# Kernel tuning notes

Hardware: AMD Instinct MI355X
Metric: run time of the kernel (lower is better)

The kernel has to match this reference:

```python
import jax, jax.numpy as jnp
import numpy as np

BINS = 30
MOMENTUM = 0.75
LOSS_WEIGHT = 1.0


def setup_inputs() -> dict:
    key = jax.random.key(0)
    k1, k2 = jax.random.split(key)
    N, C = 8192, 2048
    preds = jax.random.normal(k1, (N, C), dtype=jnp.float32)
    targets = jax.random.randint(k2, (N, C), 0, 2).astype(jnp.int32)  # binary multi-hot
    acc_sum = jnp.zeros((BINS, C), dtype=jnp.float32)  # EMA histogram state
    return {"preds": preds, "targets": targets, "acc_sum": acc_sum}


def reference(preds, targets, acc_sum):
    N, C = preds.shape
    t = targets.astype(preds.dtype)

    # gradient norm g = |sigmoid(p) - t|, detached (weights carry no grad)
    g = jnp.abs(jax.nn.sigmoid(jax.lax.stop_gradient(preds)) - t)

    # bin index: edges[i] = i/BINS, so bin = floor(g*BINS), g=1.0 -> last bin (edge[-1]+=1e-6)
    bin_idx = jnp.clip(jnp.floor(g * BINS).astype(jnp.int32), 0, BINS - 1)  # [N, C]

    # per-label histogram: counts[b, c] = #examples with bin b in column c
    cols = jnp.broadcast_to(jnp.arange(C, dtype=jnp.int32)[None, :], (N, C))
    counts = jnp.zeros((BINS, C), dtype=preds.dtype).at[bin_idx, cols].add(1.0)

    # n[c] = number of non-empty bins for label c
    n = jnp.sum(counts >= 1.0, axis=0).astype(preds.dtype)  # [C]

    # EMA update of the histogram (momentum > 0 branch)
    acc_new = MOMENTUM * acc_sum + (1.0 - MOMENTUM) * counts  # [BINS, C]

    tot = jnp.asarray(float(max(N, 1.0)), preds.dtype)
    weights = tot / acc_new[bin_idx, cols]               # gather per-element density
    weights = weights / jnp.maximum(n, 1.0)[None, :]      # normalize by #valid bins
    weights = jax.lax.stop_gradient(weights)

    # BCE with logits, elementwise: softplus-style stable form
    bce = jnp.logaddexp(0.0, preds) - preds * t
    loss = jnp.mean(weights * bce)
    return loss * LOSS_WEIGHT
```

## Files before the change

kernel.cpp:

```cpp
#include <hip/hip_runtime.h>

#define BINS  30
#define NROWS 8192
#define NCOLS 2048
#define COLS_PER_BLK 256
#define ROWS_PER_BLK 128
#define YSLICES 64

#define FIXED_SCALE 16384.0f
#define CNT_SHIFT   24
#define SUM_MASK    ((1u << CNT_SHIFT) - 1)

#define WS_PART  0
#define WS_CNT   (YSLICES * BINS * NCOLS * 4)
#define WS_BSUM  (WS_CNT + BINS * NCOLS * 4)
#define WS_BPART (WS_BSUM + BINS * NCOLS * 4)

__global__ __launch_bounds__(1024, 8) void k_main(
    const float* __restrict__ preds, const int* __restrict__ targets,
    unsigned int* __restrict__ part)
{
    __shared__ unsigned int h[BINS * COLS_PER_BLK];
    const int tid = threadIdx.x;
    for (int i = tid; i < BINS * COLS_PER_BLK; i += 1024) h[i] = 0u;
    __syncthreads();

    const int wave = tid >> 6;
    const int lane = tid & 63;
    const int colBase = blockIdx.x * COLS_PER_BLK;
    const int col0 = colBase + 4 * lane;
    const int r0   = blockIdx.y * ROWS_PER_BLK + wave * 8;

    const float4* P = (const float4*)(preds   + (size_t)r0 * NCOLS + col0);
    const int4*   T = (const int4*)  (targets + (size_t)r0 * NCOLS + col0);
    const int RV = NCOLS / 4;

    float4 pc0 = P[0], pc1 = P[RV];
    int4   tc0 = T[0], tc1 = T[RV];

    #pragma unroll
    for (int q = 0; q < 4; ++q) {
        float4 pn0, pn1;
        int4   tn0, tn1;
        if (q < 3) {
            P += 2 * RV; T += 2 * RV;
            pn0 = P[0]; pn1 = P[RV];
            tn0 = T[0]; tn1 = T[RV];
        }
        __builtin_amdgcn_sched_barrier(0);

        const float4 pb[2] = {pc0, pc1};
        const int4   tb[2] = {tc0, tc1};
        #pragma unroll
        for (int r = 0; r < 2; ++r) {
            const float pv[4] = {pb[r].x, pb[r].y, pb[r].z, pb[r].w};
            const int   tv[4] = {tb[r].x, tb[r].y, tb[r].z, tb[r].w};
            #pragma unroll
            for (int j = 0; j < 4; ++j) {
                float p  = pv[j];
                float pp = tv[j] ? -p : p;
                float e  = __expf(-fabsf(pp));
                float d  = 1.0f + e;
                float r1 = __builtin_amdgcn_rcpf(d);
                float g  = (pp >= 0.0f) ? r1 : e * r1;
                int   b  = (int)(g * 30.0f);
                b = b > (BINS - 1) ? (BINS - 1) : b;
                float bce = fmaxf(pp, 0.0f) + __logf(d);
                unsigned int pk = (1u << CNT_SHIFT)
                    | (unsigned int)(bce * FIXED_SCALE + 0.5f);
                atomicAdd(&h[b * COLS_PER_BLK + (j << 6) + lane], pk);
            }
        }
        pc0 = pn0; pc1 = pn1;
        tc0 = tn0; tc1 = tn1;
    }
    __syncthreads();

    const size_t outBase = (size_t)blockIdx.y * BINS * NCOLS + colBase;
    for (int i = tid; i < BINS * COLS_PER_BLK; i += 1024) {
        const int b = i >> 8;
        const int r = i & 255;
        const int l = r >> 2;
        const int j = r & 3;
        part[outBase + (size_t)b * NCOLS + r] = h[b * COLS_PER_BLK + (j << 6) + l];
    }
}

__global__ __launch_bounds__(256) void k_reduce(
    const unsigned int* __restrict__ part,
    float* __restrict__ cnt_f, float* __restrict__ bsum_f)
{
    const int id = blockIdx.x * 256 + threadIdx.x;
    unsigned int cnt = 0u, sm = 0u;
    #pragma unroll 16
    for (int y = 0; y < YSLICES; ++y) {
        const unsigned int v = part[(size_t)y * BINS * NCOLS + id];
        cnt += v >> CNT_SHIFT;
        sm  += v & SUM_MASK;
    }
    cnt_f[id]  = (float)cnt;
    bsum_f[id] = (float)sm * (1.0f / FIXED_SCALE);
}

__global__ __launch_bounds__(256) void k_colsum(
    const float* __restrict__ cnt_f, const float* __restrict__ bsum_f,
    const float* __restrict__ acc_sum, float* __restrict__ blockPart)
{
    __shared__ float wave_sums[4];
    const int tid = threadIdx.x;
    const int c   = blockIdx.x * 256 + tid;

    float colsum = 0.0f;
    int n = 0;
    #pragma unroll
    for (int b = 0; b < BINS; ++b) {
        const size_t gidx = (size_t)b * NCOLS + c;
        const float cnt = cnt_f[gidx];
        if (cnt >= 1.0f) {
            n += 1;
            float acc_new = 0.75f * acc_sum[gidx] + 0.25f * cnt;
            colsum += bsum_f[gidx] / acc_new;
        }
    }
    colsum /= (float)((n > 1 ? n : 1) * NCOLS);

    #pragma unroll
    for (int off = 32; off > 0; off >>= 1)
        colsum += __shfl_down(colsum, off, 64);
    if ((tid & 63) == 0) wave_sums[tid >> 6] = colsum;
    __syncthreads();
    if (tid == 0)
        blockPart[blockIdx.x] = wave_sums[0] + wave_sums[1] + wave_sums[2] + wave_sums[3];
}

__global__ void k_final(const float* __restrict__ blockPart, float* __restrict__ out)
{
    double s = 0.0;
    #pragma unroll
    for (int i = 0; i < 8; ++i) s += (double)blockPart[i];
    out[0] = (float)s;
}

extern "C" void kernel_launch(void* const* d_in, const int* in_sizes, int n_in,
                              void* d_out, int out_size, void* d_ws, size_t ws_size,
                              hipStream_t stream)
{
    const float* preds   = (const float*)d_in[0];
    const int*   targets = (const int*)d_in[1];
    const float* acc_sum = (const float*)d_in[2];

    unsigned int* part = (unsigned int*)((char*)d_ws + WS_PART);
    float* cnt_f       = (float*)((char*)d_ws + WS_CNT);
    float* bsum_f      = (float*)((char*)d_ws + WS_BSUM);
    float* blockPart   = (float*)((char*)d_ws + WS_BPART);

    dim3 gA(NCOLS / COLS_PER_BLK, NROWS / ROWS_PER_BLK);
    k_main<<<gA, 1024, 0, stream>>>(preds, targets, part);

    k_reduce<<<(BINS * NCOLS) / 256, 256, 0, stream>>>(part, cnt_f, bsum_f);

    k_colsum<<<NCOLS / 256, 256, 0, stream>>>(cnt_f, bsum_f, acc_sum, blockPart);

    k_final<<<1, 1, 0, stream>>>(blockPart, (float*)d_out);
}
```

Baseline: 187.0 us.

## Replace LDS atomic histogram with staged tile and per-column serial accumulation

Each thread now packs its bin index, count and fixed-point BCE into one word and writes it to a double-buffered shared tile. After a barrier, 256 threads each own one column and add the 8 staged values into the histogram without atomics. Blocks shrink to 512 threads and loop over 16 row tiles. The final single-thread kernel is folded into k_colsum through a last-block atomic counter, which removes one launch. The trade is a __syncthreads per tile and only half the threads doing the histogram update, in exchange for no LDS atomic contention.

```diff
diff --git a/kernel.cpp b/kernel.cpp
--- a/kernel.cpp
+++ b/kernel.cpp
@@ -10,80 +10,83 @@
 #define FIXED_SCALE 16384.0f
 #define CNT_SHIFT   24
 #define SUM_MASK    ((1u << CNT_SHIFT) - 1)
+#define PK_MASK     ((1u << (CNT_SHIFT + 1)) - 1)
 
 #define WS_PART  0
 #define WS_CNT   (YSLICES * BINS * NCOLS * 4)
 #define WS_BSUM  (WS_CNT + BINS * NCOLS * 4)
 #define WS_BPART (WS_BSUM + BINS * NCOLS * 4)
+#define WS_CTR   (WS_BPART + 8 * 4)
 
-__global__ __launch_bounds__(1024, 8) void k_main(
+__global__ __launch_bounds__(512, 4) void k_main(
     const float* __restrict__ preds, const int* __restrict__ targets,
-    unsigned int* __restrict__ part)
+    unsigned int* __restrict__ part, unsigned int* __restrict__ ctr)
 {
-    __shared__ unsigned int h[BINS * COLS_PER_BLK];
-    const int tid = threadIdx.x;
-    for (int i = tid; i < BINS * COLS_PER_BLK; i += 1024) h[i] = 0u;
-    __syncthreads();
+    __shared__ __align__(16) unsigned int H[BINS * COLS_PER_BLK];
+    __shared__ __align__(16) unsigned int Tb[2][8 * COLS_PER_BLK];
+    const int t = threadIdx.x;
+    if (blockIdx.x == 0 && blockIdx.y == 0 && t == 0) atomicExch(ctr, 0u);
+    for (int i = t; i < BINS * COLS_PER_BLK; i += 512) H[i] = 0u;
 
-    const int wave = tid >> 6;
-    const int lane = tid & 63;
+    const int wrow = t >> 6;
+    const int lane = t & 63;
     const int colBase = blockIdx.x * COLS_PER_BLK;
     const int col0 = colBase + 4 * lane;
-    const int r0   = blockIdx.y * ROWS_PER_BLK + wave * 8;
+    const int r0   = blockIdx.y * ROWS_PER_BLK + wrow;
 
     const float4* P = (const float4*)(preds   + (size_t)r0 * NCOLS + col0);
     const int4*   T = (const int4*)  (targets + (size_t)r0 * NCOLS + col0);
-    const int RV = NCOLS / 4;
+    const int RV8 = 8 * NCOLS / 4;
 
-    float4 pc0 = P[0], pc1 = P[RV];
-    int4   tc0 = T[0], tc1 = T[RV];
+    float4 pc = P[0];
+    int4   tc = T[0];
+    __syncthreads();
 
-    #pragma unroll
-    for (int q = 0; q < 4; ++q) {
-        float4 pn0, pn1;
-        int4   tn0, tn1;
-        if (q < 3) {
-            P += 2 * RV; T += 2 * RV;
-            pn0 = P[0]; pn1 = P[RV];
-            tn0 = T[0]; tn1 = T[RV];
-        }
+    #pragma unroll 2
+    for (int tile = 0; tile < 16; ++tile) {
+        float4 pn; int4 tn;
+        if (tile < 15) { P += RV8; T += RV8; pn = P[0]; tn = T[0]; }
         __builtin_amdgcn_sched_barrier(0);
 
-        const float4 pb[2] = {pc0, pc1};
-        const int4   tb[2] = {tc0, tc1};
+        const float pv[4] = {pc.x, pc.y, pc.z, pc.w};
+        const int   tv[4] = {tc.x, tc.y, tc.z, tc.w};
+        unsigned int pk[4];
         #pragma unroll
-        for (int r = 0; r < 2; ++r) {
-            const float pv[4] = {pb[r].x, pb[r].y, pb[r].z, pb[r].w};
-            const int   tv[4] = {tb[r].x, tb[r].y, tb[r].z, tb[r].w};
+        for (int j = 0; j < 4; ++j) {
+            float p  = pv[j];
+            float pp = tv[j] ? -p : p;
+            float e  = __expf(-fabsf(pp));
+            float d  = 1.0f + e;
+            float r1 = __builtin_amdgcn_rcpf(d);
+            float g  = (pp >= 0.0f) ? r1 : e * r1;
+            int   b  = (int)(g * 30.0f);
+            b = b > (BINS - 1) ? (BINS - 1) : b;
+            float bce = fmaxf(pp, 0.0f) + __logf(d);
+            pk[j] = ((unsigned int)b << 27) | (1u << CNT_SHIFT)
+                  | (unsigned int)(bce * FIXED_SCALE + 0.5f);
+        }
+        uint4 w = make_uint4(pk[0], pk[1], pk[2], pk[3]);
+        *((uint4*)&Tb[tile & 1][wrow * COLS_PER_BLK + 4 * lane]) = w;
+        __syncthreads();
+
+        if (t < COLS_PER_BLK) {
+            unsigned int v[8];
             #pragma unroll
-            for (int j = 0; j < 4; ++j) {
-                float p  = pv[j];
-                float pp = tv[j] ? -p : p;
-                float e  = __expf(-fabsf(pp));
-                float d  = 1.0f + e;
-                float r1 = __builtin_amdgcn_rcpf(d);
-                float g  = (pp >= 0.0f) ? r1 : e * r1;
-                int   b  = (int)(g * 30.0f);
-                b = b > (BINS - 1) ? (BINS - 1) : b;
-                float bce = fmaxf(pp, 0.0f) + __logf(d);
-                unsigned int pk = (1u << CNT_SHIFT)
-                    | (unsigned int)(bce * FIXED_SCALE + 0.5f);
-                atomicAdd(&h[b * COLS_PER_BLK + (j << 6) + lane], pk);
+            for (int r = 0; r < 8; ++r)
+                v[r] = Tb[tile & 1][r * COLS_PER_BLK + t];
+            #pragma unroll
+            for (int r = 0; r < 8; ++r) {
+                const int idx = (int)(v[r] >> 27) * COLS_PER_BLK + t;
+                H[idx] += v[r] & PK_MASK;
             }
         }
-        pc0 = pn0; pc1 = pn1;
-        tc0 = tn0; tc1 = tn1;
+        if (tile < 15) { pc = pn; tc = tn; }
     }
     __syncthreads();
 
     const size_t outBase = (size_t)blockIdx.y * BINS * NCOLS + colBase;
-    for (int i = tid; i < BINS * COLS_PER_BLK; i += 1024) {
-        const int b = i >> 8;
-        const int r = i & 255;
-        const int l = r >> 2;
-        const int j = r & 3;
-        part[outBase + (size_t)b * NCOLS + r] = h[b * COLS_PER_BLK + (j << 6) + l];
-    }
+    for (int i = t; i < BINS * COLS_PER_BLK; i += 512)
+        part[outBase + (size_t)(i >> 8) * NCOLS + (i & 255)] = H[i];
 }
 
 __global__ __launch_bounds__(256) void k_reduce(
@@ -104,7 +107,8 @@
 
 __global__ __launch_bounds__(256) void k_colsum(
     const float* __restrict__ cnt_f, const float* __restrict__ bsum_f,
-    const float* __restrict__ acc_sum, float* __restrict__ blockPart)
+    const float* __restrict__ acc_sum, float* __restrict__ blockPart,
+    unsigned int* __restrict__ ctr, float* __restrict__ out)
 {
     __shared__ float wave_sums[4];
     const int tid = threadIdx.x;
@@ -129,16 +133,19 @@
         colsum += __shfl_down(colsum, off, 64);
     if ((tid & 63) == 0) wave_sums[tid >> 6] = colsum;
     __syncthreads();
-    if (tid == 0)
-        blockPart[blockIdx.x] = wave_sums[0] + wave_sums[1] + wave_sums[2] + wave_sums[3];
-}
-
-__global__ void k_final(const float* __restrict__ blockPart, float* __restrict__ out)
-{
-    double s = 0.0;
-    #pragma unroll
-    for (int i = 0; i < 8; ++i) s += (double)blockPart[i];
-    out[0] = (float)s;
+    if (tid == 0) {
+        const float s = wave_sums[0] + wave_sums[1] + wave_sums[2] + wave_sums[3];
+        atomicExch(&blockPart[blockIdx.x], s);
+        __threadfence();
+        if (atomicAdd(ctr, 1u) == 7u) {
+            __threadfence();
+            double d = 0.0;
+            #pragma unroll
+            for (int i = 0; i < 8; ++i)
+                d += (double)atomicAdd(&blockPart[i], 0.0f);
+            out[0] = (float)d;
+        }
+    }
 }
 
 extern "C" void kernel_launch(void* const* d_in, const int* in_sizes, int n_in,
@@ -153,13 +160,13 @@
     float* cnt_f       = (float*)((char*)d_ws + WS_CNT);
     float* bsum_f      = (float*)((char*)d_ws + WS_BSUM);
     float* blockPart   = (float*)((char*)d_ws + WS_BPART);
+    unsigned int* ctr  = (unsigned int*)((char*)d_ws + WS_CTR);
 
     dim3 gA(NCOLS / COLS_PER_BLK, NROWS / ROWS_PER_BLK);
-    k_main<<<gA, 1024, 0, stream>>>(preds, targets, part);
+    k_main<<<gA, 512, 0, stream>>>(preds, targets, part, ctr);
 
     k_reduce<<<(BINS * NCOLS) / 256, 256, 0, stream>>>(part, cnt_f, bsum_f);
 
-    k_colsum<<<NCOLS / 256, 256, 0, stream>>>(cnt_f, bsum_f, acc_sum, blockPart);
-
-    k_final<<<1, 1, 0, stream>>>(blockPart, (float*)d_out);
+    k_colsum<<<NCOLS / 256, 256, 0, stream>>>(cnt_f, bsum_f, acc_sum,
+                                              blockPart, ctr, (float*)d_out);
 }
```

Result: faster. 183.0 us (-2.1%).
